# Kernel optimization log

Hardware: AMD Instinct MI355X
Metric: run time of the kernel (lower is better)

The kernel has to match this reference:

```python
import jax, jax.numpy as jnp
import numpy as np

NUM_EMBEDDINGS = 1024
EMBEDDING_DIM = 128
COMMITMENT_COST = 0.25
TOP_K = 3


def setup_inputs() -> dict:
    key = jax.random.key(0)
    k1, k2 = jax.random.split(key)
    inputs = jax.random.normal(k1, (32, 128, 32, 32), dtype=jnp.float32)
    embedding = jax.random.normal(k2, (NUM_EMBEDDINGS, EMBEDDING_DIM), dtype=jnp.float32)
    return {"inputs": inputs, "embedding": embedding}


def reference(inputs, embedding):
    # NCHW -> NHWC, flatten to [N, D]
    x = jnp.transpose(inputs, (0, 2, 3, 1))  # [B,H,W,D]
    input_shape = x.shape
    flat = x.reshape(-1, EMBEDDING_DIM)  # [N, D]

    # Squared L2 distances via GEMM: [N, K]
    distances = (
        jnp.sum(flat * flat, axis=1, keepdims=True)
        + jnp.sum(embedding * embedding, axis=1)
        - 2.0 * flat @ embedding.T
    )

    # top-k SMALLEST distances -> top_k of negated distances
    _, top_k_indices = jax.lax.top_k(-distances, TOP_K)  # [N, TOP_K]

    # Gather quantized vectors for all k at once: [N, TOP_K, D]
    quant_all = embedding[top_k_indices]
    # reshape per-k to input_shape -> [TOP_K, B, H, W, D]
    quant_k = jnp.transpose(quant_all, (1, 0, 2)).reshape((TOP_K,) + input_shape)

    # Torch loop leaves `encodings` = one-hot of the LAST (k-th nearest) index
    encodings = jax.nn.one_hot(top_k_indices[:, -1], NUM_EMBEDDINGS, dtype=jnp.float32)  # [N, K]

    q0 = quant_k[0]
    e_latent_loss = jnp.mean((jax.lax.stop_gradient(q0) - x) ** 2)
    loss = COMMITMENT_COST * e_latent_loss

    # Straight-through estimator
    quantized = x + jax.lax.stop_gradient(q0 - x)
    top_k_quantized = x[None] + jax.lax.stop_gradient(quant_k - x[None])  # [TOP_K,B,H,W,D]

    avg_probs = jnp.mean(encodings, axis=0)
    perplexity = jnp.exp(-jnp.sum(avg_probs * jnp.log(avg_probs + 1e-10)))

    quantized_nchw = jnp.transpose(quantized, (0, 3, 1, 2))
    return (loss, quantized_nchw, perplexity, encodings, top_k_quantized)
```

## Files before the change

kernel.cpp:

```cpp
#include <hip/hip_runtime.h>

#define BB 32
#define CC 128
#define HW 1024
#define NN 32768
#define KK 1024
#define DD 128
#define OFF_QUANT 1
#define OFF_PERP  4194305
#define OFF_ENC   4194306
#define OFF_TOPK  37748738

#define WS_PARTIALS 0
#define WS_HIST     32768
#define WS_CAND8    36864
#define WS_TOP3     1085440
#define WS_EMBBF    1609728
#define WS_ENORM    1871872

typedef __attribute__((ext_vector_type(8))) short short8;
typedef __attribute__((ext_vector_type(4))) float f32x4;
typedef __attribute__((ext_vector_type(2))) float f32x2;

__device__ __forceinline__ ushort f32_to_bf16(float v) {
    uint u = __float_as_uint(v);
    u = (u + 0x7FFFu + ((u >> 16) & 1u)) >> 16;
    return (ushort)u;
}

__global__ __launch_bounds__(256) void kP_prep(
    const float* __restrict__ in, const float* __restrict__ emb,
    ushort* __restrict__ xbf, ushort* __restrict__ embbf,
    float* __restrict__ enorm, int* __restrict__ hist)
{
    const int blk = blockIdx.x, t = threadIdx.x;
    if (blk < 128) {
        const int n  = blk * 256 + t;
        const int b  = n >> 10, hw = n & 1023;
        const float* src = in + (size_t)b * (CC * HW) + hw;
        short8* dst = (short8*)(xbf + (size_t)n * 128);
#pragma unroll 2
        for (int c0 = 0; c0 < 16; ++c0) {
            union { short8 v; ushort u[8]; } p;
#pragma unroll
            for (int j = 0; j < 8; ++j)
                p.u[j] = f32_to_bf16(src[(size_t)(c0 * 8 + j) * HW]);
            dst[c0] = p.v;
        }
    } else {
        const int rr = t >> 2, q = t & 3;
        const int row = (blk - 128) * 64 + rr;
        const float4* src = (const float4*)(emb + (size_t)row * 128 + q * 32);
        short8* dst = (short8*)(embbf + (size_t)row * 128 + q * 32);
        float nrm = 0.f;
#pragma unroll
        for (int u2 = 0; u2 < 4; ++u2) {
            float4 a = src[u2 * 2], b = src[u2 * 2 + 1];
            float f[8] = {a.x, a.y, a.z, a.w, b.x, b.y, b.z, b.w};
            union { short8 v; ushort u[8]; } p;
#pragma unroll
            for (int j = 0; j < 8; ++j) {
                nrm = fmaf(f[j], f[j], nrm);
                p.u[j] = f32_to_bf16(f[j]);
            }
            dst[u2] = p.v;
        }
        nrm += __shfl_xor(nrm, 1);
        nrm += __shfl_xor(nrm, 2);
        if (q == 0) enorm[row] = nrm;
        if (blk == 128)
            for (int i = t; i < 1024; i += 256) hist[i] = 0;
    }
}

__global__ __launch_bounds__(128) void kA2_candidates(
    const ushort* __restrict__ xbf, const ushort* __restrict__ embbf,
    const float* __restrict__ enorm, int* __restrict__ cand8)
{
    __shared__ uint4 et16[2048];
    __shared__ float enl[1024];
    uint* keybuf = (uint*)et16;

    const int t    = threadIdx.x;
    const int lane = t & 63, w = t >> 6;
    const int quad = lane >> 4, m = lane & 15;
    const int rowBase = blockIdx.x * 64;
    const int rw = rowBase + w * 32;

    for (int i = t; i < 1024; i += 128) enl[i] = enorm[i];

    short8 A[2][4];
#pragma unroll
    for (int s = 0; s < 2; ++s)
#pragma unroll
    for (int kk = 0; kk < 4; ++kk)
        A[s][kk] = *(const short8*)(xbf + (size_t)(rw + s * 16 + m) * 128 + kk * 32 + quad * 8);

    uint kq[2][4][3];
#pragma unroll
    for (int s = 0; s < 2; ++s)
#pragma unroll
    for (int i = 0; i < 4; ++i)
        kq[s][i][0] = kq[s][i][1] = kq[s][i][2] = 0xFFFFFFFFu;

    const uint4* eg = (const uint4*)embbf;

    for (int tile = 0; tile < 8; ++tile) {
        __syncthreads();
#pragma unroll
        for (int u = 0; u < 16; ++u) {
            int c = u * 128 + t;
            int row = c >> 4, kb = c & 15;
            et16[row * 16 + (kb ^ (row & 7))] = eg[(size_t)(tile * 128 + row) * 16 + kb];
        }
        __syncthreads();
#pragma unroll
        for (int sub = 0; sub < 8; ++sub) {
            f32x4 acc0 = {0.f, 0.f, 0.f, 0.f}, acc1 = {0.f, 0.f, 0.f, 0.f};
#pragma unroll
            for (int kk = 0; kk < 4; ++kk) {
                short8 B = *(const short8*)&et16[(sub * 16 + m) * 16 + ((kk * 4 + quad) ^ (m & 7))];
                acc0 = __builtin_amdgcn_mfma_f32_16x16x32_bf16(A[0][kk], B, acc0, 0, 0, 0);
                acc1 = __builtin_amdgcn_mfma_f32_16x16x32_bf16(A[1][kk], B, acc1, 0, 0, 0);
            }
            const int col = tile * 128 + sub * 16 + m;
            const float en = enl[col];
#pragma unroll
            for (int i = 0; i < 4; ++i) {
                {
                    float sc = fmaf(-2.f, acc0[i], en);
                    uint u = __float_as_uint(sc);
                    u ^= (uint)(((int)u) >> 31) | 0x80000000u;
                    uint key = (u & 0xFFFFFC00u) | (uint)col;
                    uint t0 = max(kq[0][i][0], key); kq[0][i][0] = min(kq[0][i][0], key);
                    uint t1 = max(kq[0][i][1], t0);  kq[0][i][1] = min(kq[0][i][1], t0);
                    kq[0][i][2] = min(kq[0][i][2], t1);
                }
                {
                    float sc = fmaf(-2.f, acc1[i], en);
                    uint u = __float_as_uint(sc);
                    u ^= (uint)(((int)u) >> 31) | 0x80000000u;
                    uint key = (u & 0xFFFFFC00u) | (uint)col;
                    uint t0 = max(kq[1][i][0], key); kq[1][i][0] = min(kq[1][i][0], key);
                    uint t1 = max(kq[1][i][1], t0);  kq[1][i][1] = min(kq[1][i][1], t0);
                    kq[1][i][2] = min(kq[1][i][2], t1);
                }
            }
        }
    }

    __syncthreads();
#pragma unroll
    for (int s = 0; s < 2; ++s)
#pragma unroll
    for (int i = 0; i < 4; ++i) {
        int rowl = w * 32 + s * 16 + quad * 4 + i;
#pragma unroll
        for (int j = 0; j < 3; ++j)
            keybuf[(m * 3 + j) * 65 + rowl] = kq[s][i][j];
    }
    __syncthreads();

    if (t < 64) {
        uint D[8];
#pragma unroll
        for (int s = 0; s < 8; ++s) D[s] = 0xFFFFFFFFu;
        for (int s = 0; s < 48; ++s) {
            uint k = keybuf[s * 65 + t];
            if (k < D[7]) {
                D[7] = k;
#pragma unroll
                for (int u = 7; u > 0; --u)
                    if (D[u] < D[u - 1]) { uint tmp = D[u]; D[u] = D[u - 1]; D[u - 1] = tmp; }
            }
        }
        int n = rowBase + t;
#pragma unroll
        for (int s = 0; s < 8; ++s) cand8[n * 8 + s] = (int)(D[s] & 1023u);
    }
}

__global__ __launch_bounds__(256) void kB2_refine(
    const float* __restrict__ in, const float* __restrict__ emb,
    const int* __restrict__ cand8, int* __restrict__ top3,
    int* __restrict__ hist, double* __restrict__ partials)
{
    __shared__ float x_lds[8192];
    __shared__ double lsum[64];
    const int t = threadIdx.x;
    const int rowBase = blockIdx.x * 64;
    const int b = rowBase >> 10, hw0 = rowBase & 1023;
    const float* inB = in + (size_t)b * (CC * HW) + hw0;
    for (int i = t; i < 8192; i += 256) {
        int c = i >> 6, r = i & 63;
        x_lds[c * 64 + r] = inB[c * HW + r];
    }
    __syncthreads();

    const int r = t >> 2;
    const int q = t & 3;
    const int n = rowBase + r;

    double dist[8]; int es[8];
    for (int s = 0; s < 8; ++s) {
        int e = cand8[n * 8 + s];
        es[s] = e;
        const float4* er = (const float4*)(emb + (size_t)e * DD + q * 32);
        double acc = 0.0;
#pragma unroll
        for (int u = 0; u < 8; ++u) {
            float4 ev = er[u];
            int c0 = q * 32 + u * 4;
            double a0 = (double)x_lds[(c0 + 0) * 64 + r] - (double)ev.x;
            double a1 = (double)x_lds[(c0 + 1) * 64 + r] - (double)ev.y;
            double a2 = (double)x_lds[(c0 + 2) * 64 + r] - (double)ev.z;
            double a3 = (double)x_lds[(c0 + 3) * 64 + r] - (double)ev.w;
            acc += a0 * a0 + a1 * a1 + a2 * a2 + a3 * a3;
        }
        acc += __shfl_xor(acc, 1);
        acc += __shfl_xor(acc, 2);
        dist[s] = acc;
    }

    if (q == 0) {
        bool used[8] = {false, false, false, false, false, false, false, false};
        int out_idx[3];
        double d_top1 = 0.0;
#pragma unroll
        for (int p = 0; p < 3; ++p) {
            double bd = 1.0e300; int bi = 0x7fffffff, bs = 0;
            for (int s = 0; s < 8; ++s) {
                if (used[s]) continue;
                if (dist[s] < bd || (dist[s] == bd && es[s] < bi)) {
                    bd = dist[s]; bi = es[s]; bs = s;
                }
            }
            used[bs] = true; out_idx[p] = bi;
            if (p == 0) d_top1 = bd;
        }
        top3[n * 4 + 0] = out_idx[0];
        top3[n * 4 + 1] = out_idx[1];
        top3[n * 4 + 2] = out_idx[2];
        atomicAdd(&hist[out_idx[2]], 1);
        lsum[r] = d_top1;
    }
    __syncthreads();
    if (t < 8) {
        double a = 0.0;
#pragma unroll
        for (int i = 0; i < 8; ++i) a += lsum[t * 8 + i];
        lsum[t] = a;
    }
    __syncthreads();
    if (t == 0) {
        double a = 0.0;
#pragma unroll
        for (int i = 0; i < 8; ++i) a += lsum[i];
        partials[blockIdx.x] = a;
    }
}

__global__ __launch_bounds__(256) void kEpi(
    const float* __restrict__ emb, const int* __restrict__ top3,
    const double* __restrict__ partials, const int* __restrict__ hist,
    float* __restrict__ out)
{
    const int blk = blockIdx.x, t = threadIdx.x;
    if (blk < 1024) {
        float* dst = out + OFF_QUANT;
        const int bb = blk >> 5;
        int e4[4];
#pragma unroll
        for (int v = 0; v < 4; ++v)
            e4[v] = top3[(bb * 1024 + v * 256 + t) * 4];
#pragma unroll 4
        for (int u = 0; u < 16; ++u) {
            int j = blk * 4096 + u * 256 + t;
            int c = (4 * blk + (u >> 2)) & 127;
            dst[j] = emb[e4[u & 3] * DD + c];
        }
    } else if (blk < 4096) {
        const f32x2* e2 = (const f32x2*)emb;
        f32x2* dst = (f32x2*)(out + OFF_TOPK);
#pragma unroll 4
        for (int u = 0; u < 8; ++u) {
            int j  = (blk - 1024) * 2048 + u * 256 + t;
            int c2 = j & 63;
            int n  = (j >> 6) & 32767;
            int k  = j >> 21;
            int e  = top3[n * 4 + k];
            dst[j] = e2[e * 64 + c2];
        }
    } else if (blk < 8192) {
        const int row0 = (blk - 4096) * 8;
        __shared__ int e8[8];
        if (t < 8) e8[t] = top3[(row0 + t) * 4 + 2];
        __syncthreads();
        f32x2* dst = (f32x2*)(out + OFF_ENC) + (size_t)row0 * 512;
#pragma unroll 4
        for (int u = 0; u < 16; ++u) {
            int idx = u * 256 + t;
            int e = e8[idx >> 9];
            int col = idx & 511;
            f32x2 v = {0.f, 0.f};
            if ((e >> 1) == col) v[e & 1] = 1.0f;
            dst[idx] = v;
        }
    } else {
        __shared__ double sred[256];
        sred[t] = partials[t] + partials[t + 256];
        __syncthreads();
        for (int s = 128; s > 0; s >>= 1) {
            if (t < s) sred[t] += sred[t + s];
            __syncthreads();
        }
        if (t == 0) out[0] = (float)(0.25 * sred[0] / 4194304.0);
        __syncthreads();
        double s2 = 0.0;
#pragma unroll
        for (int i = 0; i < 4; ++i) {
            double p = (double)hist[t + i * 256] * (1.0 / 32768.0);
            s2 += p * log(p + 1e-10);
        }
        sred[t] = s2;
        __syncthreads();
        for (int s = 128; s > 0; s >>= 1) {
            if (t < s) sred[t] += sred[t + s];
            __syncthreads();
        }
        if (t == 0) out[OFF_PERP] = (float)exp(-sred[0]);
    }
}

extern "C" void kernel_launch(void* const* d_in, const int* in_sizes, int n_in,
                              void* d_out, int out_size, void* d_ws, size_t ws_size,
                              hipStream_t stream)
{
    const float* in  = (const float*)d_in[0];
    const float* emb = (const float*)d_in[1];
    float* out = (float*)d_out;
    char*  ws  = (char*)d_ws;

    double* partials = (double*)(ws + WS_PARTIALS);
    int*    hist     = (int*)(ws + WS_HIST);
    int*    cand8    = (int*)(ws + WS_CAND8);
    int*    top3     = (int*)(ws + WS_TOP3);
    ushort* embbf    = (ushort*)(ws + WS_EMBBF);
    float*  enorm    = (float*)(ws + WS_ENORM);
    ushort* xbf = (ushort*)(out + OFF_TOPK + 2);

    kP_prep       <<<dim3(144), dim3(256), 0, stream>>>(in, emb, xbf, embbf, enorm, hist);
    kA2_candidates<<<dim3(512), dim3(128), 0, stream>>>(xbf, embbf, enorm, cand8);
    kB2_refine    <<<dim3(512), dim3(256), 0, stream>>>(in, emb, cand8, top3, hist, partials);
    kEpi          <<<dim3(8193), dim3(256), 0, stream>>>(emb, top3, partials, hist, out);
}
```

Measured before the change: 328.5 us.

## Fuse candidate search and refinement into one kernel, convert inputs inline

```diff
diff --git a/kernel.cpp b/kernel.cpp
--- a/kernel.cpp
+++ b/kernel.cpp
@@ -13,7 +13,6 @@
 
 #define WS_PARTIALS 0
 #define WS_HIST     32768
-#define WS_CAND8    36864
 #define WS_TOP3     1085440
 #define WS_EMBBF    1609728
 #define WS_ENORM    1871872
@@ -28,136 +27,131 @@
     return (ushort)u;
 }
 
-__global__ __launch_bounds__(256) void kP_prep(
-    const float* __restrict__ in, const float* __restrict__ emb,
-    ushort* __restrict__ xbf, ushort* __restrict__ embbf,
+__global__ __launch_bounds__(256) void kP_emb(
+    const float* __restrict__ emb, ushort* __restrict__ embbf,
     float* __restrict__ enorm, int* __restrict__ hist)
 {
     const int blk = blockIdx.x, t = threadIdx.x;
-    if (blk < 128) {
-        const int n  = blk * 256 + t;
-        const int b  = n >> 10, hw = n & 1023;
-        const float* src = in + (size_t)b * (CC * HW) + hw;
-        short8* dst = (short8*)(xbf + (size_t)n * 128);
-#pragma unroll 2
-        for (int c0 = 0; c0 < 16; ++c0) {
-            union { short8 v; ushort u[8]; } p;
-#pragma unroll
-            for (int j = 0; j < 8; ++j)
-                p.u[j] = f32_to_bf16(src[(size_t)(c0 * 8 + j) * HW]);
-            dst[c0] = p.v;
-        }
-    } else {
-        const int rr = t >> 2, q = t & 3;
-        const int row = (blk - 128) * 64 + rr;
-        const float4* src = (const float4*)(emb + (size_t)row * 128 + q * 32);
-        short8* dst = (short8*)(embbf + (size_t)row * 128 + q * 32);
-        float nrm = 0.f;
-#pragma unroll
-        for (int u2 = 0; u2 < 4; ++u2) {
-            float4 a = src[u2 * 2], b = src[u2 * 2 + 1];
-            float f[8] = {a.x, a.y, a.z, a.w, b.x, b.y, b.z, b.w};
-            union { short8 v; ushort u[8]; } p;
-#pragma unroll
-            for (int j = 0; j < 8; ++j) {
-                nrm = fmaf(f[j], f[j], nrm);
-                p.u[j] = f32_to_bf16(f[j]);
-            }
-            dst[u2] = p.v;
-        }
-        nrm += __shfl_xor(nrm, 1);
-        nrm += __shfl_xor(nrm, 2);
-        if (q == 0) enorm[row] = nrm;
-        if (blk == 128)
-            for (int i = t; i < 1024; i += 256) hist[i] = 0;
-    }
-}
-
-__global__ __launch_bounds__(128) void kA2_candidates(
-    const ushort* __restrict__ xbf, const ushort* __restrict__ embbf,
-    const float* __restrict__ enorm, int* __restrict__ cand8)
+    const int rr = t >> 2, q = t & 3;
+    const int row = blk * 64 + rr;
+    const float4* src = (const float4*)(emb + (size_t)row * 128 + q * 32);
+    short8* dst = (short8*)(embbf + (size_t)row * 128 + q * 32);
+    float nrm = 0.f;
+#pragma unroll
+    for (int u2 = 0; u2 < 4; ++u2) {
+        float4 a = src[u2 * 2], b2 = src[u2 * 2 + 1];
+        float f[8] = {a.x, a.y, a.z, a.w, b2.x, b2.y, b2.z, b2.w};
+        union { short8 v; ushort u[8]; } p;
+#pragma unroll
+        for (int j = 0; j < 8; ++j) {
+            nrm = fmaf(f[j], f[j], nrm);
+            p.u[j] = f32_to_bf16(f[j]);
+        }
+        dst[u2] = p.v;
+    }
+    nrm += __shfl_xor(nrm, 1);
+    nrm += __shfl_xor(nrm, 2);
+    if (q == 0) enorm[row] = nrm;
+    if (blk == 0)
+        for (int i = t; i < 1024; i += 256) hist[i] = 0;
+}
+
+__global__ __launch_bounds__(256) void kA2B(
+    const float* __restrict__ in, const float* __restrict__ emb,
+    const ushort* __restrict__ embbf, const float* __restrict__ enorm,
+    int* __restrict__ top3, int* __restrict__ hist, double* __restrict__ partials)
 {
-    __shared__ uint4 et16[2048];
+    __shared__ union {
+        float xs[128 * 66];
+        uint4 et16[2048];
+    } sh;
     __shared__ float enl[1024];
-    uint* keybuf = (uint*)et16;
-
-    const int t    = threadIdx.x;
+    __shared__ double lsum[64];
+    __shared__ int cbuf[512];
+
+    const int t = threadIdx.x;
     const int lane = t & 63, w = t >> 6;
     const int quad = lane >> 4, m = lane & 15;
     const int rowBase = blockIdx.x * 64;
-    const int rw = rowBase + w * 32;
-
-    for (int i = t; i < 1024; i += 128) enl[i] = enorm[i];
-
-    short8 A[2][4];
-#pragma unroll
-    for (int s = 0; s < 2; ++s)
-#pragma unroll
-    for (int kk = 0; kk < 4; ++kk)
-        A[s][kk] = *(const short8*)(xbf + (size_t)(rw + s * 16 + m) * 128 + kk * 32 + quad * 8);
-
-    uint kq[2][4][3];
-#pragma unroll
-    for (int s = 0; s < 2; ++s)
+    const int b = rowBase >> 10, hw0 = rowBase & 1023;
+    const float* inB = in + (size_t)b * (CC * HW) + hw0;
+
+    for (int i = t; i < 1024; i += 256) enl[i] = enorm[i];
+
+    short8 A[4];
+    {
+        const int ra = w * 16 + m;
+#pragma unroll
+        for (int kk = 0; kk < 4; ++kk) {
+            union { short8 v; ushort u[8]; } p;
+#pragma unroll
+            for (int j = 0; j < 8; ++j)
+                p.u[j] = f32_to_bf16(inB[(size_t)(kk * 32 + quad * 8 + j) * HW + ra]);
+            A[kk] = p.v;
+        }
+    }
+
+    uint kq[4][3];
 #pragma unroll
     for (int i = 0; i < 4; ++i)
-        kq[s][i][0] = kq[s][i][1] = kq[s][i][2] = 0xFFFFFFFFu;
+        kq[i][0] = kq[i][1] = kq[i][2] = 0xFFFFFFFFu;
 
     const uint4* eg = (const uint4*)embbf;
 
     for (int tile = 0; tile < 8; ++tile) {
         __syncthreads();
 #pragma unroll
-        for (int u = 0; u < 16; ++u) {
-            int c = u * 128 + t;
+        for (int u = 0; u < 8; ++u) {
+            int c = u * 256 + t;
             int row = c >> 4, kb = c & 15;
-            et16[row * 16 + (kb ^ (row & 7))] = eg[(size_t)(tile * 128 + row) * 16 + kb];
-        }
-        __syncthreads();
-#pragma unroll
-        for (int sub = 0; sub < 8; ++sub) {
+            sh.et16[row * 16 + (kb ^ (row & 7))] = eg[(size_t)(tile * 128 + row) * 16 + kb];
+        }
+        __syncthreads();
+#pragma unroll
+        for (int sp = 0; sp < 4; ++sp) {
             f32x4 acc0 = {0.f, 0.f, 0.f, 0.f}, acc1 = {0.f, 0.f, 0.f, 0.f};
 #pragma unroll
             for (int kk = 0; kk < 4; ++kk) {
-                short8 B = *(const short8*)&et16[(sub * 16 + m) * 16 + ((kk * 4 + quad) ^ (m & 7))];
-                acc0 = __builtin_amdgcn_mfma_f32_16x16x32_bf16(A[0][kk], B, acc0, 0, 0, 0);
-                acc1 = __builtin_amdgcn_mfma_f32_16x16x32_bf16(A[1][kk], B, acc1, 0, 0, 0);
+                int sl = (kk * 4 + quad) ^ (m & 7);
+                short8 B0 = *(const short8*)&sh.et16[((sp * 2)     * 16 + m) * 16 + sl];
+                short8 B1 = *(const short8*)&sh.et16[((sp * 2 + 1) * 16 + m) * 16 + sl];
+                acc0 = __builtin_amdgcn_mfma_f32_16x16x32_bf16(A[kk], B0, acc0, 0, 0, 0);
+                acc1 = __builtin_amdgcn_mfma_f32_16x16x32_bf16(A[kk], B1, acc1, 0, 0, 0);
             }
-            const int col = tile * 128 + sub * 16 + m;
-            const float en = enl[col];
+            const int col0 = tile * 128 + (sp * 2) * 16 + m;
+            const float en0 = enl[col0], en1 = enl[col0 + 16];
 #pragma unroll
             for (int i = 0; i < 4; ++i) {
                 {
-                    float sc = fmaf(-2.f, acc0[i], en);
-                    uint u = __float_as_uint(sc);
-                    u ^= (uint)(((int)u) >> 31) | 0x80000000u;
-                    uint key = (u & 0xFFFFFC00u) | (uint)col;
-                    uint t0 = max(kq[0][i][0], key); kq[0][i][0] = min(kq[0][i][0], key);
-                    uint t1 = max(kq[0][i][1], t0);  kq[0][i][1] = min(kq[0][i][1], t0);
-                    kq[0][i][2] = min(kq[0][i][2], t1);
+                    float sc = fmaf(-2.f, acc0[i], en0);
+                    uint u_ = __float_as_uint(sc);
+                    u_ ^= (uint)(((int)u_) >> 31) | 0x80000000u;
+                    uint key = (u_ & 0xFFFFFC00u) | (uint)col0;
+                    uint t0 = max(kq[i][0], key); kq[i][0] = min(kq[i][0], key);
+                    uint t1 = max(kq[i][1], t0);  kq[i][1] = min(kq[i][1], t0);
+                    kq[i][2] = min(kq[i][2], t1);
                 }
                 {
-                    float sc = fmaf(-2.f, acc1[i], en);
-                    uint u = __float_as_uint(sc);
-                    u ^= (uint)(((int)u) >> 31) | 0x80000000u;
-                    uint key = (u & 0xFFFFFC00u) | (uint)col;
-                    uint t0 = max(kq[1][i][0], key); kq[1][i][0] = min(kq[1][i][0], key);
-                    uint t1 = max(kq[1][i][1], t0);  kq[1][i][1] = min(kq[1][i][1], t0);
-                    kq[1][i][2] = min(kq[1][i][2], t1);
+                    float sc = fmaf(-2.f, acc1[i], en1);
+                    uint u_ = __float_as_uint(sc);
+                    u_ ^= (uint)(((int)u_) >> 31) | 0x80000000u;
+                    uint key = (u_ & 0xFFFFFC00u) | (uint)(col0 + 16);
+                    uint t0 = max(kq[i][0], key); kq[i][0] = min(kq[i][0], key);
+                    uint t1 = max(kq[i][1], t0);  kq[i][1] = min(kq[i][1], t0);
+                    kq[i][2] = min(kq[i][2], t1);
                 }
             }
         }
     }
 
     __syncthreads();
-#pragma unroll
-    for (int s = 0; s < 2; ++s)
+    uint* keybuf = (uint*)sh.et16;
 #pragma unroll
     for (int i = 0; i < 4; ++i) {
-        int rowl = w * 32 + s * 16 + quad * 4 + i;
+        int rowl = w * 16 + quad * 4 + i;
 #pragma unroll
         for (int j = 0; j < 3; ++j)
-            keybuf[(m * 3 + j) * 65 + rowl] = kq[s][i][j];
+            keybuf[(m * 3 + j) * 65 + rowl] = kq[i][j];
     }
     __syncthreads();
 
@@ -174,26 +168,14 @@
                     if (D[u] < D[u - 1]) { uint tmp = D[u]; D[u] = D[u - 1]; D[u - 1] = tmp; }
             }
         }
-        int n = rowBase + t;
-#pragma unroll
-        for (int s = 0; s < 8; ++s) cand8[n * 8 + s] = (int)(D[s] & 1023u);
-    }
-}
-
-__global__ __launch_bounds__(256) void kB2_refine(
-    const float* __restrict__ in, const float* __restrict__ emb,
-    const int* __restrict__ cand8, int* __restrict__ top3,
-    int* __restrict__ hist, double* __restrict__ partials)
-{
-    __shared__ float x_lds[8192];
-    __shared__ double lsum[64];
-    const int t = threadIdx.x;
-    const int rowBase = blockIdx.x * 64;
-    const int b = rowBase >> 10, hw0 = rowBase & 1023;
-    const float* inB = in + (size_t)b * (CC * HW) + hw0;
+#pragma unroll
+        for (int s = 0; s < 8; ++s) cbuf[t * 8 + s] = (int)(D[s] & 1023u);
+    }
+    __syncthreads();
+
     for (int i = t; i < 8192; i += 256) {
-        int c = i >> 6, r = i & 63;
-        x_lds[c * 64 + r] = inB[c * HW + r];
+        int c = i >> 6, r2 = i & 63;
+        sh.xs[c * 66 + r2] = inB[(size_t)c * HW + r2];
     }
     __syncthreads();
 
@@ -202,8 +184,9 @@
     const int n = rowBase + r;
 
     double dist[8]; int es[8];
+#pragma unroll
     for (int s = 0; s < 8; ++s) {
-        int e = cand8[n * 8 + s];
+        int e = cbuf[r * 8 + s];
         es[s] = e;
         const float4* er = (const float4*)(emb + (size_t)e * DD + q * 32);
         double acc = 0.0;
@@ -211,10 +194,10 @@
         for (int u = 0; u < 8; ++u) {
             float4 ev = er[u];
             int c0 = q * 32 + u * 4;
-            double a0 = (double)x_lds[(c0 + 0) * 64 + r] - (double)ev.x;
-            double a1 = (double)x_lds[(c0 + 1) * 64 + r] - (double)ev.y;
-            double a2 = (double)x_lds[(c0 + 2) * 64 + r] - (double)ev.z;
-            double a3 = (double)x_lds[(c0 + 3) * 64 + r] - (double)ev.w;
+            double a0 = (double)sh.xs[(c0 + 0) * 66 + r] - (double)ev.x;
+            double a1 = (double)sh.xs[(c0 + 1) * 66 + r] - (double)ev.y;
+            double a2 = (double)sh.xs[(c0 + 2) * 66 + r] - (double)ev.z;
+            double a3 = (double)sh.xs[(c0 + 3) * 66 + r] - (double)ev.w;
             acc += a0 * a0 + a1 * a1 + a2 * a2 + a3 * a3;
         }
         acc += __shfl_xor(acc, 1);
@@ -223,19 +206,21 @@
     }
 
     if (q == 0) {
-        bool used[8] = {false, false, false, false, false, false, false, false};
+        unsigned usedm = 0;
         int out_idx[3];
         double d_top1 = 0.0;
 #pragma unroll
         for (int p = 0; p < 3; ++p) {
             double bd = 1.0e300; int bi = 0x7fffffff, bs = 0;
+#pragma unroll
             for (int s = 0; s < 8; ++s) {
-                if (used[s]) continue;
+                if ((usedm >> s) & 1u) continue;
                 if (dist[s] < bd || (dist[s] == bd && es[s] < bi)) {
                     bd = dist[s]; bi = es[s]; bs = s;
                 }
             }
-            used[bs] = true; out_idx[p] = bi;
+            usedm |= (1u << bs);
+            out_idx[p] = bi;
             if (p == 0) d_top1 = bd;
         }
         top3[n * 4 + 0] = out_idx[0];
@@ -248,14 +233,14 @@
     if (t < 8) {
         double a = 0.0;
 #pragma unroll
-        for (int i = 0; i < 8; ++i) a += lsum[t * 8 + i];
+        for (int i2 = 0; i2 < 8; ++i2) a += lsum[t * 8 + i2];
         lsum[t] = a;
     }
     __syncthreads();
     if (t == 0) {
         double a = 0.0;
 #pragma unroll
-        for (int i = 0; i < 8; ++i) a += lsum[i];
+        for (int i2 = 0; i2 < 8; ++i2) a += lsum[i2];
         partials[blockIdx.x] = a;
     }
 }
@@ -265,19 +250,32 @@
     const double* __restrict__ partials, const int* __restrict__ hist,
     float* __restrict__ out)
 {
+    __shared__ union {
+        float cols[4][1024];
+        int e8[8];
+        double sred[256];
+    } sh;
     const int blk = blockIdx.x, t = threadIdx.x;
     if (blk < 1024) {
         float* dst = out + OFF_QUANT;
         const int bb = blk >> 5;
+        const int c0 = (4 * blk) & 127;
+#pragma unroll
+        for (int k = 0; k < 4; ++k) {
+            int e = k * 256 + t;
+            float4 f4 = *(const float4*)(emb + (size_t)e * DD + c0);
+            sh.cols[0][e] = f4.x; sh.cols[1][e] = f4.y;
+            sh.cols[2][e] = f4.z; sh.cols[3][e] = f4.w;
+        }
         int e4[4];
 #pragma unroll
         for (int v = 0; v < 4; ++v)
             e4[v] = top3[(bb * 1024 + v * 256 + t) * 4];
+        __syncthreads();
 #pragma unroll 4
         for (int u = 0; u < 16; ++u) {
             int j = blk * 4096 + u * 256 + t;
-            int c = (4 * blk + (u >> 2)) & 127;
-            dst[j] = emb[e4[u & 3] * DD + c];
+            dst[j] = sh.cols[u >> 2][e4[u & 3]];
         }
     } else if (blk < 4096) {
         const f32x2* e2 = (const f32x2*)emb;
@@ -293,28 +291,26 @@
         }
     } else if (blk < 8192) {
         const int row0 = (blk - 4096) * 8;
-        __shared__ int e8[8];
-        if (t < 8) e8[t] = top3[(row0 + t) * 4 + 2];
+        if (t < 8) sh.e8[t] = top3[(row0 + t) * 4 + 2];
         __syncthreads();
         f32x2* dst = (f32x2*)(out + OFF_ENC) + (size_t)row0 * 512;
 #pragma unroll 4
         for (int u = 0; u < 16; ++u) {
             int idx = u * 256 + t;
-            int e = e8[idx >> 9];
+            int e = sh.e8[idx >> 9];
             int col = idx & 511;
             f32x2 v = {0.f, 0.f};
             if ((e >> 1) == col) v[e & 1] = 1.0f;
             dst[idx] = v;
         }
     } else {
-        __shared__ double sred[256];
-        sred[t] = partials[t] + partials[t + 256];
+        sh.sred[t] = partials[t] + partials[t + 256];
         __syncthreads();
         for (int s = 128; s > 0; s >>= 1) {
-            if (t < s) sred[t] += sred[t + s];
+            if (t < s) sh.sred[t] += sh.sred[t + s];
             __syncthreads();
         }
-        if (t == 0) out[0] = (float)(0.25 * sred[0] / 4194304.0);
+        if (t == 0) out[0] = (float)(0.25 * sh.sred[0] / 4194304.0);
         __syncthreads();
         double s2 = 0.0;
 #pragma unroll
@@ -322,13 +318,13 @@
             double p = (double)hist[t + i * 256] * (1.0 / 32768.0);
             s2 += p * log(p + 1e-10);
         }
-        sred[t] = s2;
+        sh.sred[t] = s2;
         __syncthreads();
         for (int s = 128; s > 0; s >>= 1) {
-            if (t < s) sred[t] += sred[t + s];
+            if (t < s) sh.sred[t] += sh.sred[t + s];
             __syncthreads();
         }
-        if (t == 0) out[OFF_PERP] = (float)exp(-sred[0]);
+        if (t == 0) out[OFF_PERP] = (float)exp(-sh.sred[0]);
     }
 }
 
@@ -343,14 +339,11 @@
 
     double* partials = (double*)(ws + WS_PARTIALS);
     int*    hist     = (int*)(ws + WS_HIST);
-    int*    cand8    = (int*)(ws + WS_CAND8);
     int*    top3     = (int*)(ws + WS_TOP3);
     ushort* embbf    = (ushort*)(ws + WS_EMBBF);
     float*  enorm    = (float*)(ws + WS_ENORM);
-    ushort* xbf = (ushort*)(out + OFF_TOPK + 2);
-
-    kP_prep       <<<dim3(144), dim3(256), 0, stream>>>(in, emb, xbf, embbf, enorm, hist);
-    kA2_candidates<<<dim3(512), dim3(128), 0, stream>>>(xbf, embbf, enorm, cand8);
-    kB2_refine    <<<dim3(512), dim3(256), 0, stream>>>(in, emb, cand8, top3, hist, partials);
-    kEpi          <<<dim3(8193), dim3(256), 0, stream>>>(emb, top3, partials, hist, out);
-}
+
+    kP_emb<<<dim3(16),   dim3(256), 0, stream>>>(emb, embbf, enorm, hist);
+    kA2B  <<<dim3(512),  dim3(256), 0, stream>>>(in, emb, embbf, enorm, top3, hist, partials);
+    kEpi  <<<dim3(8193), dim3(256), 0, stream>>>(emb, top3, partials, hist, out);
+}
```

Measured after the change: 279.8 us. -14.8%, faster.
